# Kernel tuning notes

Measured on AMD Instinct MI355X. Metric: run time of the kernel, lower is better.

## Reference

```python
import jax, jax.numpy as jnp
import numpy as np

N_NODES = 100000
N_EDGES = 1600000
IN_CH = 128
HEADS = 4
OUT_CH = 32
NEG_SLOPE = 0.2
EPS = 1e-10


def setup_inputs() -> dict:
    key = jax.random.key(0)
    k1, k2, k3, k4 = jax.random.split(key, 4)
    x = jax.random.normal(k1, (N_NODES, IN_CH), dtype=jnp.float32)
    edge_index = jax.random.randint(k2, (2, N_EDGES), 0, N_NODES, dtype=jnp.int64)
    # small scale keeps exp(-leakyrelu(score)) numerically tame
    W = jax.random.normal(k3, (IN_CH, HEADS * OUT_CH), dtype=jnp.float32) * 0.05
    attention = jax.random.normal(k4, (HEADS, 2 * OUT_CH), dtype=jnp.float32) * 0.05
    bias = jnp.zeros((HEADS * OUT_CH,), dtype=jnp.float32)
    return {"x": x, "edge_index": edge_index, "W": W, "attention": attention, "bias": bias}


def reference(x, edge_index, W, attention, bias):
    N = x.shape[0]
    H, two_o = attention.shape
    O = two_o // 2
    # shared fc_src == fc_tgt (in_channels is an int in the original)
    h = (x @ W).reshape(N, H, O)  # [N, H, O]
    # attention vector splits over the concat [h_src || h_tgt]
    a_src, a_tgt = attention[:, :O], attention[:, O:]
    s_src = jnp.einsum('nho,ho->nh', h, a_src)  # [N, H]
    s_tgt = jnp.einsum('nho,ho->nh', h, a_tgt)  # [N, H]
    src, tgt = edge_index[0], edge_index[1]
    score = s_src[src] + s_tgt[tgt]  # [E, H]
    # NOTE: original applies exp to the NEGATED LeakyReLU output
    e = jnp.exp(-jax.nn.leaky_relu(score, NEG_SLOPE))  # [E, H]
    # numerator: sum_j e_ij * h_src[j] scattered to target nodes
    num = jax.ops.segment_sum(e[:, :, None] * h[src], tgt, num_segments=N)  # [N, H, O]
    den = jax.ops.segment_sum(e, tgt, num_segments=N)  # [N, H]
    out = num / jnp.clip(den, EPS, None)[:, :, None]
    out = out.reshape(N, H * O)  # concat=True
    return out + bias
```

## Files before the change

kernel.cpp:

```cpp
#include <hip/hip_runtime.h>
#include <stdint.h>


#define NN 100000
#define EE 1600000
#define INCH 128
#define HO 128
#define HEADS 4
#define OUTC 32

#define BSH 8
#define NBUCK ((NN + 255) >> BSH)
#define CAPBK 5120
#define CHA 4096
#define ABLK ((EE + CHA - 1) / CHA)

typedef unsigned short ushort_t;
typedef unsigned int uint_t;
typedef __attribute__((ext_vector_type(8))) short bf16x8;
typedef __attribute__((ext_vector_type(4))) float f32x4;

__device__ __forceinline__ float bfl(uint_t u) { return __uint_as_float(u << 16); }
__device__ __forceinline__ float bfh(uint_t u) { return __uint_as_float(u & 0xffff0000u); }
__device__ __forceinline__ uint_t f2bf(float f) {
    uint_t u = __float_as_uint(f);
    u = (u + 0x7fffu + ((u >> 16) & 1u)) >> 16;
    return u;
}

__global__ __launch_bounds__(256) void prepW_k(const float* __restrict__ W,
                                               ushort_t* __restrict__ gWtHi,
                                               ushort_t* __restrict__ gWtLo) {
    const int gidx = blockIdx.x * 256 + threadIdx.x;
    const int col = gidx & 127;
    const int k = gidx >> 7;
    const float v = W[k * 128 + col];
    const uint_t h = f2bf(v);
    const uint_t lo = f2bf(v - bfl(h));
    gWtHi[col * 128 + k] = (ushort_t)h;
    gWtLo[col * 128 + k] = (ushort_t)lo;
}

__global__ __launch_bounds__(256) void gemm_h(const float* __restrict__ x,
                                              const ushort_t* __restrict__ gWtHi,
                                              const ushort_t* __restrict__ gWtLo,
                                              const float* __restrict__ att,
                                              ushort_t* __restrict__ hb,
                                              float* __restrict__ s_src,
                                              float* __restrict__ s_tgt) {
    __shared__ __align__(16) char smem[16384];
    ushort_t* xHi  = (ushort_t*)smem;
    ushort_t* xLo  = (ushort_t*)(smem + 8192);
    const int tid = threadIdx.x;
    const int row0 = blockIdx.x * 32;

    const int lane = tid & 63;
    const int w = tid >> 6;
    const int l15 = lane & 15;
    const int g = lane >> 4;
    const int swz = (l15 & 7) << 4;

    bf16x8 bh[2][4], bl[2][4];
    {
        const ushort_t* pH = gWtHi + (size_t)(w * 32 + l15) * 128 + g * 8;
        const ushort_t* pL = gWtLo + (size_t)(w * 32 + l15) * 128 + g * 8;
#pragma unroll
        for (int ntl = 0; ntl < 2; ++ntl)
#pragma unroll
            for (int ks = 0; ks < 4; ++ks) {
                bh[ntl][ks] = *(const bf16x8*)(pH + ntl * 16 * 128 + ks * 32);
                bl[ntl][ks] = *(const bf16x8*)(pL + ntl * 16 * 128 + ks * 32);
            }
    }

    {
        const float4* x4 = (const float4*)(x + (size_t)row0 * INCH);
#pragma unroll
        for (int j = 0; j < 4; ++j) {
            const int i = tid + 256 * j;
            const int row = i >> 5;
            const int k4 = i & 31;
            const float4 v = x4[i];
            const uint_t h0 = f2bf(v.x), h1 = f2bf(v.y), h2 = f2bf(v.z), h3 = f2bf(v.w);
            const uint_t l0 = f2bf(v.x - bfl(h0));
            const uint_t l1 = f2bf(v.y - bfl(h1));
            const uint_t l2 = f2bf(v.z - bfl(h2));
            const uint_t l3 = f2bf(v.w - bfl(h3));
            const int byteOff = (row * 256 + k4 * 8) ^ ((row & 7) << 4);
            *(uint2*)((char*)xHi + byteOff) = make_uint2(h0 | (h1 << 16), h2 | (h3 << 16));
            *(uint2*)((char*)xLo + byteOff) = make_uint2(l0 | (l1 << 16), l2 | (l3 << 16));
        }
    }
    __syncthreads();

    f32x4 acc[2][2] = {};
#pragma unroll
    for (int ks = 0; ks < 4; ++ks) {
        const int kb = ks * 64 + g * 16;
        const bf16x8 a0h = *(const bf16x8*)((char*)xHi + ((l15 * 256 + kb) ^ swz));
        const bf16x8 a1h = *(const bf16x8*)((char*)xHi + (((16 + l15) * 256 + kb) ^ swz));
        const bf16x8 a0l = *(const bf16x8*)((char*)xLo + ((l15 * 256 + kb) ^ swz));
        const bf16x8 a1l = *(const bf16x8*)((char*)xLo + (((16 + l15) * 256 + kb) ^ swz));
        acc[0][0] = __builtin_amdgcn_mfma_f32_16x16x32_bf16(a0h, bh[0][ks], acc[0][0], 0, 0, 0);
        acc[0][1] = __builtin_amdgcn_mfma_f32_16x16x32_bf16(a0h, bh[1][ks], acc[0][1], 0, 0, 0);
        acc[1][0] = __builtin_amdgcn_mfma_f32_16x16x32_bf16(a1h, bh[0][ks], acc[1][0], 0, 0, 0);
        acc[1][1] = __builtin_amdgcn_mfma_f32_16x16x32_bf16(a1h, bh[1][ks], acc[1][1], 0, 0, 0);
        acc[0][0] = __builtin_amdgcn_mfma_f32_16x16x32_bf16(a0h, bl[0][ks], acc[0][0], 0, 0, 0);
        acc[0][1] = __builtin_amdgcn_mfma_f32_16x16x32_bf16(a0h, bl[1][ks], acc[0][1], 0, 0, 0);
        acc[1][0] = __builtin_amdgcn_mfma_f32_16x16x32_bf16(a1h, bl[0][ks], acc[1][0], 0, 0, 0);
        acc[1][1] = __builtin_amdgcn_mfma_f32_16x16x32_bf16(a1h, bl[1][ks], acc[1][1], 0, 0, 0);
        acc[0][0] = __builtin_amdgcn_mfma_f32_16x16x32_bf16(a0l, bh[0][ks], acc[0][0], 0, 0, 0);
        acc[0][1] = __builtin_amdgcn_mfma_f32_16x16x32_bf16(a0l, bh[1][ks], acc[0][1], 0, 0, 0);
        acc[1][0] = __builtin_amdgcn_mfma_f32_16x16x32_bf16(a1l, bh[0][ks], acc[1][0], 0, 0, 0);
        acc[1][1] = __builtin_amdgcn_mfma_f32_16x16x32_bf16(a1l, bh[1][ks], acc[1][1], 0, 0, 0);
    }

#pragma unroll
    for (int mt = 0; mt < 2; ++mt)
#pragma unroll
        for (int ntl = 0; ntl < 2; ++ntl) {
            const int col = w * 32 + ntl * 16 + l15;
#pragma unroll
            for (int r = 0; r < 4; ++r) {
                const int row = row0 + mt * 16 + g * 4 + r;
                hb[(size_t)row * HO + col] = (ushort_t)f2bf(acc[mt][ntl][r]);
            }
        }

    const float cs0 = att[w * 64 + l15];
    const float cs1 = att[w * 64 + 16 + l15];
    const float ct0 = att[w * 64 + 32 + l15];
    const float ct1 = att[w * 64 + 48 + l15];
#pragma unroll
    for (int mt = 0; mt < 2; ++mt)
#pragma unroll
        for (int r = 0; r < 4; ++r) {
            float ps = acc[mt][0][r] * cs0 + acc[mt][1][r] * cs1;
            float pt = acc[mt][0][r] * ct0 + acc[mt][1][r] * ct1;
#pragma unroll
            for (int d = 1; d < 16; d <<= 1) {
                ps += __shfl_xor(ps, d, 64);
                pt += __shfl_xor(pt, d, 64);
            }
            if (l15 == 0) {
                const int row = row0 + mt * 16 + g * 4 + r;
                s_src[row * 4 + w] = ps;
                s_tgt[row * 4 + w] = pt;
            }
        }
}

__global__ __launch_bounds__(512) void bucketA_k(const int* __restrict__ ei,
                                                 int* __restrict__ gcur,
                                                 uint_t* __restrict__ grec) {
    __shared__ int hist[NBUCK];
    __shared__ int gbase[NBUCK];
    __shared__ int lcur[NBUCK];
    const int tid = threadIdx.x;
    const int e0 = blockIdx.x * CHA;
    const int cnt = min(CHA, EE - e0);

    for (int b = tid; b < NBUCK; b += 512) hist[b] = 0;
    __syncthreads();
    for (int i = tid; i < cnt; i += 512)
        atomicAdd(&hist[ei[EE + e0 + i] >> BSH], 1);
    __syncthreads();
    for (int b = tid; b < NBUCK; b += 512) {
        const int h = hist[b];
        gbase[b] = b * CAPBK + (h ? atomicAdd(&gcur[b], h) : 0);
        lcur[b] = 0;
    }
    __syncthreads();
    for (int i = tid; i < cnt; i += 512) {
        const int src = ei[e0 + i];
        const int tgt = ei[EE + e0 + i];
        const int b = tgt >> BSH;
        const int p = atomicAdd(&lcur[b], 1);
        grec[gbase[b] + p] = (uint_t)src | ((uint_t)(tgt & 255) << 17);
    }
}

__global__ __launch_bounds__(1024) void bucketB_k(const int* __restrict__ bucketCnt,
                                                  const uint_t* __restrict__ grec,
                                                  int2* __restrict__ offs2,
                                                  int* __restrict__ sorted_src) {
    __shared__ int cur[256];
    __shared__ int scn[256];
    __shared__ uint_t sbuf[CAPBK];
    const int tid = threadIdx.x;
    const int b = blockIdx.x;
    const int n0 = b << BSH;
    const int nn = min(256, NN - n0);
    const int R0 = b * CAPBK;
    const int cnt = min(bucketCnt[b], CAPBK);

    if (tid < 256) cur[tid] = 0;
    __syncthreads();
    uint_t r0v = 0xFFFFFFFFu, r1v = 0xFFFFFFFFu, r2v = 0xFFFFFFFFu,
           r3v = 0xFFFFFFFFu, r4v = 0xFFFFFFFFu;
    {
        int i = tid;
        if (i < cnt) { r0v = grec[R0 + i]; atomicAdd(&cur[r0v >> 17], 1); } i += 1024;
        if (i < cnt) { r1v = grec[R0 + i]; atomicAdd(&cur[r1v >> 17], 1); } i += 1024;
        if (i < cnt) { r2v = grec[R0 + i]; atomicAdd(&cur[r2v >> 17], 1); } i += 1024;
        if (i < cnt) { r3v = grec[R0 + i]; atomicAdd(&cur[r3v >> 17], 1); } i += 1024;
        if (i < cnt) { r4v = grec[R0 + i]; atomicAdd(&cur[r4v >> 17], 1); }
    }
    __syncthreads();
    int v = 0;
    if (tid < 256) { v = cur[tid]; scn[tid] = v; }
    __syncthreads();
#pragma unroll
    for (int off = 1; off < 256; off <<= 1) {
        int u = (tid < 256 && tid >= off) ? scn[tid - off] : 0;
        __syncthreads();
        if (tid < 256) scn[tid] += u;
        __syncthreads();
    }
    if (tid < 256) {
        const int ex = scn[tid] - v;
        cur[tid] = ex;
        if (tid < nn) offs2[n0 + tid] = make_int2(R0 + ex, R0 + ex + v);
    }
    __syncthreads();
    if (r0v != 0xFFFFFFFFu) sbuf[atomicAdd(&cur[r0v >> 17], 1)] = r0v;
    if (r1v != 0xFFFFFFFFu) sbuf[atomicAdd(&cur[r1v >> 17], 1)] = r1v;
    if (r2v != 0xFFFFFFFFu) sbuf[atomicAdd(&cur[r2v >> 17], 1)] = r2v;
    if (r3v != 0xFFFFFFFFu) sbuf[atomicAdd(&cur[r3v >> 17], 1)] = r3v;
    if (r4v != 0xFFFFFFFFu) sbuf[atomicAdd(&cur[r4v >> 17], 1)] = r4v;
    __syncthreads();
    for (int i = tid; i < cnt; i += 1024)
        sorted_src[R0 + i] = (int)(sbuf[i] & 0x1FFFF);
}

__device__ __forceinline__ void gstep(int pe, int hd, int c0, float st,
                                      const int* __restrict__ sorted_src,
                                      const float* __restrict__ s_src,
                                      const ushort_t* __restrict__ hb,
                                      float ax[8], float& wsum) {
    const int s = sorted_src[pe];
    float sc = s_src[s * 4 + hd] + st;
    sc = fmaxf(sc, 0.2f * sc);
    const float w = __expf(-sc);
    const uint4 v = *(const uint4*)(hb + (size_t)s * HO + c0);
    ax[0] = fmaf(w, bfl(v.x), ax[0]); ax[1] = fmaf(w, bfh(v.x), ax[1]);
    ax[2] = fmaf(w, bfl(v.y), ax[2]); ax[3] = fmaf(w, bfh(v.y), ax[3]);
    ax[4] = fmaf(w, bfl(v.z), ax[4]); ax[5] = fmaf(w, bfh(v.z), ax[5]);
    ax[6] = fmaf(w, bfl(v.w), ax[6]); ax[7] = fmaf(w, bfh(v.w), ax[7]);
    wsum += w;
}

__global__ __launch_bounds__(256) void gather_k(const int2* __restrict__ offs2,
                                                const int* __restrict__ sorted_src,
                                                const float* __restrict__ s_src,
                                                const float* __restrict__ s_tgt,
                                                const ushort_t* __restrict__ hb,
                                                const float* __restrict__ bias,
                                                float* __restrict__ out) {
    const int n = blockIdx.x * 4 + (threadIdx.x >> 6);
    const int l = threadIdx.x & 63;
    const int eg = l >> 4;
    const int ch16 = l & 15;
    const int hd = ch16 >> 2;
    const int c0 = ch16 * 8;
    const int2 pr = offs2[n];
    const int pend = pr.y;
    const float st = s_tgt[n * 4 + hd];
    float ax[8] = {};
    float wsum = 0.f;
    int p = pr.x;
    for (; p + 16 <= pend; p += 16) {
        gstep(p + eg,      hd, c0, st, sorted_src, s_src, hb, ax, wsum);
        gstep(p + 4 + eg,  hd, c0, st, sorted_src, s_src, hb, ax, wsum);
        gstep(p + 8 + eg,  hd, c0, st, sorted_src, s_src, hb, ax, wsum);
        gstep(p + 12 + eg, hd, c0, st, sorted_src, s_src, hb, ax, wsum);
    }
    if (p < pend) {
        if (p + eg < pend)      gstep(p + eg,      hd, c0, st, sorted_src, s_src, hb, ax, wsum);
        if (p + 4 + eg < pend)  gstep(p + 4 + eg,  hd, c0, st, sorted_src, s_src, hb, ax, wsum);
        if (p + 8 + eg < pend)  gstep(p + 8 + eg,  hd, c0, st, sorted_src, s_src, hb, ax, wsum);
        if (p + 12 + eg < pend) gstep(p + 12 + eg, hd, c0, st, sorted_src, s_src, hb, ax, wsum);
    }
#pragma unroll
    for (int d = 16; d <= 32; d <<= 1) {
#pragma unroll
        for (int j = 0; j < 8; ++j) ax[j] += __shfl_xor(ax[j], d, 64);
        wsum += __shfl_xor(wsum, d, 64);
    }
    if (eg == 0) {
        const float inv = 1.f / fmaxf(wsum, 1e-10f);
        const float4 b0 = *(const float4*)(bias + c0);
        const float4 b1 = *(const float4*)(bias + c0 + 4);
        float4 o0, o1;
        o0.x = fmaf(ax[0], inv, b0.x); o0.y = fmaf(ax[1], inv, b0.y);
        o0.z = fmaf(ax[2], inv, b0.z); o0.w = fmaf(ax[3], inv, b0.w);
        o1.x = fmaf(ax[4], inv, b1.x); o1.y = fmaf(ax[5], inv, b1.y);
        o1.z = fmaf(ax[6], inv, b1.z); o1.w = fmaf(ax[7], inv, b1.w);
        *(float4*)(out + (size_t)n * HO + c0) = o0;
        *(float4*)(out + (size_t)n * HO + c0 + 4) = o1;
    }
}

extern "C" void kernel_launch(void* const* d_in, const int* in_sizes, int n_in,
                              void* d_out, int out_size, void* d_ws, size_t ws_size,
                              hipStream_t stream) {
    const float* x    = (const float*)d_in[0];
    const int*   ei   = (const int*)d_in[1];
    const float* W    = (const float*)d_in[2];
    const float* att  = (const float*)d_in[3];
    const float* bias = (const float*)d_in[4];
    float* out = (float*)d_out;

    char* ws = (char*)d_ws;
    const size_t HB_B  = (size_t)NN * HO * 2;
    const size_t SS_B  = (size_t)NBUCK * CAPBK * 4;
    const size_t GR_B  = (size_t)NBUCK * CAPBK * 4;
    const size_t S_B   = (size_t)NN * HEADS * 4;
    const size_t OF_B  = ((size_t)NN * 8 + 15) & ~15ull;
    const size_t GC_B  = ((size_t)NBUCK * 4 + 15) & ~15ull;
    const size_t WT_B  = 32768;

    size_t o = 0;
    ushort_t* hb         = (ushort_t*)(ws + o); o += HB_B;
    int*      sorted_src = (int*)(ws + o); o += SS_B;
    uint_t*   grec       = (uint_t*)(ws + o); o += GR_B;
    float*    ssrc       = (float*)(ws + o); o += S_B;
    float*    stgt       = (float*)(ws + o); o += S_B;
    int2*     offs2      = (int2*)(ws + o); o += OF_B;
    int*      gcur       = (int*)(ws + o); o += GC_B;
    ushort_t* gWtHi      = (ushort_t*)(ws + o); o += WT_B;
    ushort_t* gWtLo      = (ushort_t*)(ws + o); o += WT_B;

    (void)hipMemsetAsync(gcur, 0, GC_B, stream);

    prepW_k<<<64, 256, 0, stream>>>(W, gWtHi, gWtLo);
    gemm_h<<<NN / 32, 256, 0, stream>>>(x, gWtHi, gWtLo, att,
                                        hb, ssrc, stgt);
    bucketA_k<<<ABLK, 512, 0, stream>>>(ei, gcur, grec);
    bucketB_k<<<NBUCK, 1024, 0, stream>>>(gcur, grec, offs2, sorted_src);
    gather_k<<<NN / 4, 256, 0, stream>>>(offs2, sorted_src, ssrc, stgt,
                                         hb, bias, out);
}
```

Measured before the change: 247.8 us.

## Precompute per-edge attention weights in bucket sort, stream them in gather

Moves the per-edge score, leaky-relu and exp computation from the gather kernel into the bucket-sort scatter pass, writing a float4 of per-head weights per sorted edge. Gather then reads one contiguous weight vector instead of doing a random s_src lookup and an exp. The gather loop is also restructured into a single 32-edge unrolled loop with per-step bounds checks. This adds a 16-byte-per-edge write and read of the new weight array, and bucketB now performs random s_src reads of its own.

Result: slower. 268.0 us (+8.2%).

```diff
diff --git a/kernel.cpp b/kernel.cpp
--- a/kernel.cpp
+++ b/kernel.cpp
@@ -26,6 +26,9 @@
     uint_t u = __float_as_uint(f);
     u = (u + 0x7fffu + ((u >> 16) & 1u)) >> 16;
     return u;
+}
+__device__ __forceinline__ float att_w(float sc) {
+    return __expf(-(sc > 0.f ? sc : 0.2f * sc));
 }
 
 __global__ __launch_bounds__(256) void prepW_k(const float* __restrict__ W,
@@ -182,8 +185,11 @@
 
 __global__ __launch_bounds__(1024) void bucketB_k(const int* __restrict__ bucketCnt,
                                                   const uint_t* __restrict__ grec,
+                                                  const float* __restrict__ s_src,
+                                                  const float* __restrict__ s_tgt,
                                                   int2* __restrict__ offs2,
-                                                  int* __restrict__ sorted_src) {
+                                                  int* __restrict__ sorted_src,
+                                                  float4* __restrict__ wgt) {
     __shared__ int cur[256];
     __shared__ int scn[256];
     __shared__ uint_t sbuf[CAPBK];
@@ -229,19 +235,31 @@
     if (r3v != 0xFFFFFFFFu) sbuf[atomicAdd(&cur[r3v >> 17], 1)] = r3v;
     if (r4v != 0xFFFFFFFFu) sbuf[atomicAdd(&cur[r4v >> 17], 1)] = r4v;
     __syncthreads();
-    for (int i = tid; i < cnt; i += 1024)
-        sorted_src[R0 + i] = (int)(sbuf[i] & 0x1FFFF);
-}
-
-__device__ __forceinline__ void gstep(int pe, int hd, int c0, float st,
+    for (int i = tid; i < cnt; i += 1024) {
+        const uint_t r = sbuf[i];
+        const int src = (int)(r & 0x1FFFF);
+        const int tl = (int)(r >> 17);
+        sorted_src[R0 + i] = src;
+        const float4 ss = *(const float4*)(s_src + src * 4);
+        const float4 st = *(const float4*)(s_tgt + (n0 + tl) * 4);
+        float4 wv;
+        wv.x = att_w(ss.x + st.x);
+        wv.y = att_w(ss.y + st.y);
+        wv.z = att_w(ss.z + st.z);
+        wv.w = att_w(ss.w + st.w);
+        wgt[R0 + i] = wv;
+    }
+}
+
+__device__ __forceinline__ void gstep(int pe, int hd, int c0,
                                       const int* __restrict__ sorted_src,
-                                      const float* __restrict__ s_src,
+                                      const float4* __restrict__ wgt,
                                       const ushort_t* __restrict__ hb,
                                       float ax[8], float& wsum) {
     const int s = sorted_src[pe];
-    float sc = s_src[s * 4 + hd] + st;
-    sc = fmaxf(sc, 0.2f * sc);
-    const float w = __expf(-sc);
+    const float4 wq = wgt[pe];
+    const float w = (hd & 2) ? ((hd & 1) ? wq.w : wq.z)
+                             : ((hd & 1) ? wq.y : wq.x);
     const uint4 v = *(const uint4*)(hb + (size_t)s * HO + c0);
     ax[0] = fmaf(w, bfl(v.x), ax[0]); ax[1] = fmaf(w, bfh(v.x), ax[1]);
     ax[2] = fmaf(w, bfl(v.y), ax[2]); ax[3] = fmaf(w, bfh(v.y), ax[3]);
@@ -252,8 +270,7 @@
 
 __global__ __launch_bounds__(256) void gather_k(const int2* __restrict__ offs2,
                                                 const int* __restrict__ sorted_src,
-                                                const float* __restrict__ s_src,
-                                                const float* __restrict__ s_tgt,
+                                                const float* __restrict__ wgt,
                                                 const ushort_t* __restrict__ hb,
                                                 const float* __restrict__ bias,
                                                 float* __restrict__ out) {
@@ -265,21 +282,16 @@
     const int c0 = ch16 * 8;
     const int2 pr = offs2[n];
     const int pend = pr.y;
-    const float st = s_tgt[n * 4 + hd];
+    const float4* wgt4 = (const float4*)wgt;
     float ax[8] = {};
     float wsum = 0.f;
-    int p = pr.x;
-    for (; p + 16 <= pend; p += 16) {
-        gstep(p + eg,      hd, c0, st, sorted_src, s_src, hb, ax, wsum);
-        gstep(p + 4 + eg,  hd, c0, st, sorted_src, s_src, hb, ax, wsum);
-        gstep(p + 8 + eg,  hd, c0, st, sorted_src, s_src, hb, ax, wsum);
-        gstep(p + 12 + eg, hd, c0, st, sorted_src, s_src, hb, ax, wsum);
-    }
-    if (p < pend) {
-        if (p + eg < pend)      gstep(p + eg,      hd, c0, st, sorted_src, s_src, hb, ax, wsum);
-        if (p + 4 + eg < pend)  gstep(p + 4 + eg,  hd, c0, st, sorted_src, s_src, hb, ax, wsum);
-        if (p + 8 + eg < pend)  gstep(p + 8 + eg,  hd, c0, st, sorted_src, s_src, hb, ax, wsum);
-        if (p + 12 + eg < pend) gstep(p + 12 + eg, hd, c0, st, sorted_src, s_src, hb, ax, wsum);
+    for (int p = pr.x; p < pend; p += 32) {
+#pragma unroll
+        for (int j = 0; j < 8; ++j) {
+            const int pe = p + j * 4 + eg;
+            if (pe < pend)
+                gstep(pe, hd, c0, sorted_src, wgt4, hb, ax, wsum);
+        }
     }
 #pragma unroll
     for (int d = 16; d <= 32; d <<= 1) {
@@ -315,6 +327,7 @@
     const size_t HB_B  = (size_t)NN * HO * 2;
     const size_t SS_B  = (size_t)NBUCK * CAPBK * 4;
     const size_t GR_B  = (size_t)NBUCK * CAPBK * 4;
+    const size_t WG_B  = (size_t)NBUCK * CAPBK * 16;
     const size_t S_B   = (size_t)NN * HEADS * 4;
     const size_t OF_B  = ((size_t)NN * 8 + 15) & ~15ull;
     const size_t GC_B  = ((size_t)NBUCK * 4 + 15) & ~15ull;
@@ -324,6 +337,7 @@
     ushort_t* hb         = (ushort_t*)(ws + o); o += HB_B;
     int*      sorted_src = (int*)(ws + o); o += SS_B;
     uint_t*   grec       = (uint_t*)(ws + o); o += GR_B;
+    float4*   wgt        = (float4*)(ws + o); o += WG_B;
     float*    ssrc       = (float*)(ws + o); o += S_B;
     float*    stgt       = (float*)(ws + o); o += S_B;
     int2*     offs2      = (int2*)(ws + o); o += OF_B;
@@ -337,7 +351,8 @@
     gemm_h<<<NN / 32, 256, 0, stream>>>(x, gWtHi, gWtLo, att,
                                         hb, ssrc, stgt);
     bucketA_k<<<ABLK, 512, 0, stream>>>(ei, gcur, grec);
-    bucketB_k<<<NBUCK, 1024, 0, stream>>>(gcur, grec, offs2, sorted_src);
-    gather_k<<<NN / 4, 256, 0, stream>>>(offs2, sorted_src, ssrc, stgt,
+    bucketB_k<<<NBUCK, 1024, 0, stream>>>(gcur, grec, ssrc, stgt,
+                                          offs2, sorted_src, wgt);
+    gather_k<<<NN / 4, 256, 0, stream>>>(offs2, sorted_src, (const float*)wgt,
                                          hb, bias, out);
 }
```
